# Optimization experiments

Measured on AMD Instinct MI355X. Metric: run time of the kernel, lower is better.

Reference implementation:

```python
import jax, jax.numpy as jnp
import numpy as np

N_NODES = 8192
GNN_DIM = 512
N_FEAT = 64
N_ITER = 4


def setup_inputs() -> dict:
    key = jax.random.key(0)
    ks = jax.random.split(key, 8)
    scale = 1.0 / np.sqrt(GNN_DIM)
    return {
        "labels": jax.random.normal(ks[0], (N_NODES, GNN_DIM), dtype=jnp.float32),
        "adj": jax.random.uniform(ks[1], (N_NODES, N_NODES), dtype=jnp.float32),
        "features": jax.random.normal(ks[2], (N_FEAT,), dtype=jnp.float32),
        "W_self": jax.random.normal(ks[3], (GNN_DIM, GNN_DIM), dtype=jnp.float32) * scale,
        "b_self": jax.random.normal(ks[4], (GNN_DIM,), dtype=jnp.float32) * scale,
        "W_neigh": jax.random.normal(ks[5], (GNN_DIM, GNN_DIM), dtype=jnp.float32) * scale,
        "W_fc": jax.random.normal(ks[6], (1, GNN_DIM + N_FEAT), dtype=jnp.float32) * scale,
        "b_fc": jax.random.normal(ks[7], (1,), dtype=jnp.float32) * scale,
    }


def reference(labels, adj, features, W_self, b_self, W_neigh, W_fc, b_fc):
    x = labels  # [N, D]
    for _ in range(N_ITER):
        acc = adj @ x                                   # [N, D] neighbor aggregation
        x = jax.nn.relu(x @ W_self.T + b_self + acc @ W_neigh.T)
    pooled = jnp.mean(x, axis=0)                        # [D]
    z = jnp.concatenate([pooled, features]) @ W_fc.T + b_fc  # [1]
    return jax.nn.sigmoid(z)
```

## Files before the change

kernel.cpp:

```cpp
#include <hip/hip_runtime.h>

typedef __bf16 bf16;
typedef bf16 bf16x8 __attribute__((ext_vector_type(8)));
typedef bf16 bf16x4 __attribute__((ext_vector_type(4)));
typedef float f32x4 __attribute__((ext_vector_type(4)));
typedef int i32x4 __attribute__((ext_vector_type(4)));
typedef unsigned int u32;
typedef unsigned int u32x4 __attribute__((ext_vector_type(4)));
typedef unsigned char u8;
typedef unsigned long long u64;

constexpr int NN = 8192;
constexpr int DD = 512;
constexpr size_t PSZB = (size_t)NN * DD * 2;
constexpr size_t PSZE = (size_t)NN * DD;
constexpr int NS = 4;

static __device__ inline bf16x8 cvt8(const float* __restrict__ p) {
  f32x4 a = *(const f32x4*)p;
  f32x4 b = *(const f32x4*)(p + 4);
  bf16x8 r;
  r[0] = (bf16)a[0]; r[1] = (bf16)a[1]; r[2] = (bf16)a[2]; r[3] = (bf16)a[3];
  r[4] = (bf16)b[0]; r[5] = (bf16)b[1]; r[6] = (bf16)b[2]; r[7] = (bf16)b[3];
  return r;
}

static __device__ inline u32 pk4_i8(f32x4 v) {
  u32 b0 = (u32)((int)__builtin_rintf(v[0])) & 255u;
  u32 b1 = (u32)((int)__builtin_rintf(v[1])) & 255u;
  u32 b2 = (u32)((int)__builtin_rintf(v[2])) & 255u;
  u32 b3 = (u32)((int)__builtin_rintf(v[3])) & 255u;
  return b0 | (b1 << 8) | (b2 << 16) | (b3 << 24);
}

#define GLDS(g, l) __builtin_amdgcn_global_load_lds( \
    (const __attribute__((address_space(1))) unsigned int*)(const void*)(g), \
    (__attribute__((address_space(3))) unsigned int*)(void*)(l), 16, 0, 0)


__global__ __launch_bounds__(256) void convert_w_kernel(
    const float* __restrict__ a, const float* __restrict__ b,
    bf16* __restrict__ ao, bf16* __restrict__ bo, float* __restrict__ pooled) {
  int tid = (int)threadIdx.x;
  if (blockIdx.x == 0) {
    pooled[tid] = 0.f;
    pooled[tid + 256] = 0.f;
  }
  int i8 = ((int)blockIdx.x * 256 + tid) * 8;
  if (i8 < DD * DD) {
    *(bf16x8*)&ao[i8] = cvt8(a + i8);
  } else {
    int j = i8 - DD * DD;
    *(bf16x8*)&bo[j] = cvt8(b + j);
  }
}

__global__ __launch_bounds__(256) void convert_adj_kernel(
    const float* __restrict__ a, u8* __restrict__ o) {
  size_t i16 = ((size_t)blockIdx.x * 256 + threadIdx.x) * 16;
  const float* p = a + i16;
  u32x4 w;
#pragma unroll
  for (int q = 0; q < 4; ++q) {
    f32x4 v = *(const f32x4*)(p + 4 * q);
    v *= 127.f;
    w[q] = pk4_i8(v);
  }
  *(u32x4*)(o + i16) = w;
}

__global__ __launch_bounds__(256) void convert_x_kernel(
    const float* __restrict__ src, bf16* __restrict__ xb, u8* __restrict__ xbT8) {
  __shared__ __align__(16) float tile[64][68];
  const int tid = (int)threadIdx.x;
  const int r0 = (int)blockIdx.x * 64;
  const int c0 = (int)blockIdx.y * 64;
#pragma unroll
  for (int p = 0; p < 4; ++p) {
    int row = p * 16 + (tid >> 4);
    int col = (tid & 15) * 4;
    *(f32x4*)&tile[row][col] = *(const f32x4*)&src[(size_t)(r0 + row) * DD + c0 + col];
  }
  __syncthreads();
#pragma unroll
  for (int p = 0; p < 4; ++p) {
    int row = p * 16 + (tid >> 4);
    int col = (tid & 15) * 4;
    f32x4 v = *(const f32x4*)&tile[row][col];
    bf16x4 o;
    o[0] = (bf16)v[0]; o[1] = (bf16)v[1]; o[2] = (bf16)v[2]; o[3] = (bf16)v[3];
    *(bf16x4*)&xb[(size_t)(r0 + row) * DD + c0 + col] = o;
  }
  {
    int c = tid >> 2;
    int rp = (tid & 3) * 16;
    u32x4 w;
#pragma unroll
    for (int q = 0; q < 4; ++q) {
      f32x4 v;
#pragma unroll
      for (int j = 0; j < 4; ++j) v[j] = tile[rp + 4 * q + j][c] * 16.f;
      w[q] = pk4_i8(v);
    }
    *(u32x4*)&xbT8[(size_t)(c0 + c) * NN + r0 + rp] = w;
  }
}


__device__ __forceinline__ void stage_half8(const u8* __restrict__ g, int grow0, int k0b,
                                            u8* smbase, int wave, int lane) {
  int row = grow0 + wave * 16 + (lane >> 2);
  int col = k0b + (((lane & 3) ^ ((lane >> 2) & 3)) << 4);
  GLDS(g + (size_t)row * NN + col, smbase + wave * 1024);
}

__global__ __launch_bounds__(512, 4)
void gemm1_kernel(const u8* __restrict__ adjb, const u8* __restrict__ xbT8,
                  bf16* __restrict__ pbase) {
  __shared__ __align__(16) u8 sm[49152];
  const int bid  = (int)blockIdx.x;
  const int xcd  = bid & 7;
  const int p    = bid >> 3;
  const int s    = xcd >> 1;
  const int cb   = xcd & 1;
  const int prow0 = p * 128;
  const int bcol0 = cb * 256;
  const int kb    = s * 2048;
  bf16* __restrict__ P = pbase + (size_t)s * PSZE;

  const int tid  = (int)threadIdx.x;
  const int lane = tid & 63;
  const int wave = tid >> 6;
  const int wr   = wave >> 2;
  const int wc   = wave & 3;
  const int fr   = lane & 15, fq = lane >> 4;

  i32x4 acc[4][4] = {};

#define A_OFF(par) ((par) * 24576)
#define B_OFF(par) ((par) * 24576 + 8192)
#define STAGE_A(tile, par) \
  stage_half8(adjb, prow0, kb + ((tile) & 31) * 64, sm + A_OFF(par), wave, lane)
#define STAGE_B(tile, half, par) \
  stage_half8(xbT8, bcol0 + (half) * 128, kb + ((tile) & 31) * 64, \
              sm + B_OFF(par) + (half) * 8192, wave, lane)
#define BARRIER() __builtin_amdgcn_s_barrier(); __builtin_amdgcn_sched_barrier(0)

  STAGE_B(0, 0, 0); STAGE_B(0, 1, 0); STAGE_A(0, 0);
  STAGE_B(1, 0, 1); STAGE_B(1, 1, 1);

  i32x4 bvp[4], afp[2];

#define LOAD_B(par)                                                        \
  _Pragma("unroll") for (int n = 0; n < 4; ++n) {                          \
    int rowl = wc * 64 + n * 16 + fr;                                      \
    int slot = fq ^ (rowl & 3);                                            \
    bvp[n] = *(const i32x4*)&sm[B_OFF(par) + rowl * 64 + slot * 16];       \
  }
#define LOAD_A2(qb, par)                                                   \
  _Pragma("unroll") for (int j = 0; j < 2; ++j) {                          \
    int rowl = wr * 64 + ((qb) + j) * 16 + fr;                             \
    int slot = fq ^ (rowl & 3);                                            \
    afp[j] = *(const i32x4*)&sm[A_OFF(par) + rowl * 64 + slot * 16];       \
  }
#define HMFMA(qb)                                                          \
  __builtin_amdgcn_s_setprio(1);                                           \
  _Pragma("unroll") for (int j = 0; j < 2; ++j)                            \
  _Pragma("unroll") for (int n = 0; n < 4; ++n)                            \
    acc[(qb) + j][n] = __builtin_amdgcn_mfma_i32_16x16x64_i8(              \
        afp[j], bvp[n], acc[(qb) + j][n], 0, 0, 0);                        \
  __builtin_amdgcn_s_setprio(0);

  int par = 0;
  for (int t = 0; t < 32; ++t, par ^= 1) {
    asm volatile("s_waitcnt vmcnt(2)" ::: "memory");
    BARRIER();
    LOAD_B(par);
    LOAD_A2(0, par);
    STAGE_A(t + 1, par ^ 1);
    HMFMA(0);
    BARRIER();
    LOAD_A2(2, par);
    STAGE_B(t + 2, 0, par);
    STAGE_B(t + 2, 1, par);
    HMFMA(2);
  }

#pragma unroll
  for (int m = 0; m < 4; ++m)
#pragma unroll
    for (int n = 0; n < 4; ++n)
#pragma unroll
      for (int r = 0; r < 4; ++r) {
        int row = prow0 + wr * 64 + m * 16 + fq * 4 + r;
        int col = bcol0 + wc * 64 + n * 16 + fr;
        P[(size_t)row * DD + col] = (bf16)(float)acc[m][n][r];
      }
#undef A_OFF
#undef B_OFF
#undef STAGE_A
#undef STAGE_B
#undef LOAD_B
#undef LOAD_A2
#undef HMFMA
#undef BARRIER
}

__global__ __launch_bounds__(1024, 4)
void gemm2_kernel(const bf16* __restrict__ wsb, const bf16* __restrict__ wnb,
                  bf16* __restrict__ xb, const bf16* __restrict__ pbase,
                  const float* __restrict__ bself, u8* __restrict__ xbT8,
                  float* __restrict__ pooled, int dopool,
                  float alpha, float inv_bn) {
  __shared__ __align__(16) char smem[139264];
  const int tid  = (int)threadIdx.x;
  const int lane = tid & 63;
  const int wave = tid >> 6;
  const int n0 = (int)blockIdx.x * 32;
  const int fr = lane & 15, fq = lane >> 4;
  const int srow = lane >> 3;
  const int scol = ((lane & 7) ^ (srow & 7)) * 8;
  const int fnode = tid >> 3, fks = tid & 7;

  f32x4 acc[2][2] = {};

  {
    bf16* la = (bf16*)smem;
#pragma unroll
    for (int c = 0; c < 4; ++c) {
      int chunk = wave * 4 + c;
      GLDS(wsb + (size_t)(chunk * 8 + srow) * DD + scol, &la[chunk * 512]);
    }
    if (wave < 4)
      GLDS(xb + (size_t)(n0 + wave * 8 + srow) * DD + scol,
           &((bf16*)(smem + 131072))[wave * 512]);
  }
  asm volatile("s_waitcnt vmcnt(0)" ::: "memory");
  __builtin_amdgcn_s_barrier();

  for (int t = 0; t < 16; ++t) {
    const int par = t & 1;
    bf16* la = (bf16*)(smem + par * 65536);
    bf16* lb = (bf16*)(smem + 131072 + par * 4096);

    bf16x8 fv0, fv1, fv2, fv3;
    bool fold = false;
    if (t < 15) {
      const int tn = t + 1, prn = tn >> 3, k0n = (tn & 7) * 64;
      const bf16* __restrict__ An = prn ? wnb : wsb;
      bf16* lan = (bf16*)(smem + (par ^ 1) * 65536);
#pragma unroll
      for (int c = 0; c < 4; ++c) {
        int chunk = wave * 4 + c;
        GLDS(An + (size_t)(chunk * 8 + srow) * DD + k0n + scol, &lan[chunk * 512]);
      }
      if (prn == 0) {
        if (wave < 4)
          GLDS(xb + (size_t)(n0 + wave * 8 + srow) * DD + k0n + scol,
               &((bf16*)(smem + 131072 + (par ^ 1) * 4096))[wave * 512]);
      } else if (tid < 256) {
        fold = true;
        const bf16* p0 = pbase + (size_t)(n0 + fnode) * DD + k0n + fks * 8;
        fv0 = *(const bf16x8*)(p0);
        fv1 = *(const bf16x8*)(p0 + PSZE);
        fv2 = *(const bf16x8*)(p0 + 2 * PSZE);
        fv3 = *(const bf16x8*)(p0 + 3 * PSZE);
      }
    }

    bf16x8 af[2][2], bv[2][2];
#pragma unroll
    for (int kk = 0; kk < 2; ++kk) {
#pragma unroll
      for (int m = 0; m < 2; ++m) {
        int rowl = wave * 32 + m * 16 + fr;
        int slot = (kk * 4 + fq) ^ (rowl & 7);
        af[kk][m] = *(const bf16x8*)&la[rowl * 64 + slot * 8];
      }
#pragma unroll
      for (int n = 0; n < 2; ++n) {
        int rowl = n * 16 + fr;
        int slot = (kk * 4 + fq) ^ (rowl & 7);
        bv[kk][n] = *(const bf16x8*)&lb[rowl * 64 + slot * 8];
      }
    }
#pragma unroll
    for (int kk = 0; kk < 2; ++kk)
#pragma unroll
      for (int m = 0; m < 2; ++m)
#pragma unroll
        for (int n = 0; n < 2; ++n)
          acc[m][n] = __builtin_amdgcn_mfma_f32_16x16x32_bf16(af[kk][m], bv[kk][n], acc[m][n], 0, 0, 0);

    if (fold) {
      bf16x8 o;
#pragma unroll
      for (int j = 0; j < 8; ++j)
        o[j] = (bf16)(((float)fv0[j] + (float)fv1[j] + (float)fv2[j] + (float)fv3[j]) * alpha);
      *(bf16x8*)&((bf16*)(smem + 131072 + (par ^ 1) * 4096))[fnode * 64 + (fks ^ (fnode & 7)) * 8] = o;
    }

    asm volatile("s_waitcnt vmcnt(0) lgkmcnt(0)" ::: "memory");
    __builtin_amdgcn_s_barrier();
  }

  if (dopool) {
#pragma unroll
    for (int m = 0; m < 2; ++m)
#pragma unroll
      for (int r = 0; r < 4; ++r) {
        int d = wave * 32 + m * 16 + fq * 4 + r;
        float b = bself[d];
        float v0 = acc[m][0][r] + b, v1 = acc[m][1][r] + b;
        float sv = (v0 > 0.f ? v0 : 0.f) + (v1 > 0.f ? v1 : 0.f);
        sv += __shfl_xor(sv, 1);
        sv += __shfl_xor(sv, 2);
        sv += __shfl_xor(sv, 4);
        sv += __shfl_xor(sv, 8);
        if (fr == 0) atomicAdd(&pooled[d], sv);
      }
    return;
  }

  bf16* lds_t = (bf16*)smem;
  u8*   lds8  = (u8*)(smem + 40960);
#pragma unroll
  for (int m = 0; m < 2; ++m)
#pragma unroll
    for (int n = 0; n < 2; ++n)
#pragma unroll
      for (int r = 0; r < 4; ++r) {
        int d = wave * 32 + m * 16 + fq * 4 + r;
        int node = n * 16 + fr;
        float v = acc[m][n][r] + bself[d];
        v = v > 0.f ? v : 0.f;
        lds_t[node * 520 + d] = (bf16)v;
        lds8[d * 32 + node] = (u8)(int)__builtin_rintf(fminf(v * inv_bn, 127.f));
      }
  __syncthreads();
  {
    int node = tid >> 5;
    int dc = (tid & 31) * 16;
    bf16x8 v0 = *(const bf16x8*)&lds_t[node * 520 + dc];
    bf16x8 v1 = *(const bf16x8*)&lds_t[node * 520 + dc + 8];
    *(bf16x8*)&xb[(size_t)(n0 + node) * DD + dc] = v0;
    *(bf16x8*)&xb[(size_t)(n0 + node) * DD + dc + 8] = v1;
  }
  {
    int d = tid >> 1, half = tid & 1;
    u32x4 w = *(const u32x4*)&lds8[d * 32 + half * 16];
    *(u32x4*)&xbT8[(size_t)d * NN + n0 + half * 16] = w;
  }
}


__global__ __launch_bounds__(64) void final_kernel(
    const float* __restrict__ pooled, const float* __restrict__ features,
    const float* __restrict__ wfc, const float* __restrict__ bfc,
    float* __restrict__ out) {
  const int t = (int)threadIdx.x;
  float s = 0.f;
  for (int i = t; i < DD + 64; i += 64) {
    float v = (i < DD) ? pooled[i] * (1.0f / (float)NN) : features[i - DD];
    s += v * wfc[i];
  }
#pragma unroll
  for (int off = 32; off > 0; off >>= 1) s += __shfl_down(s, off);
  if (t == 0) {
    float z = s + bfc[0];
    out[0] = 1.0f / (1.0f + expf(-z));
  }
}


extern "C" void kernel_launch(void* const* d_in, const int* in_sizes, int n_in,
                              void* d_out, int out_size, void* d_ws, size_t ws_size,
                              hipStream_t stream) {
  const float* labels   = (const float*)d_in[0];
  const float* adj      = (const float*)d_in[1];
  const float* features = (const float*)d_in[2];
  const float* W_self   = (const float*)d_in[3];
  const float* b_self   = (const float*)d_in[4];
  const float* W_neigh  = (const float*)d_in[5];
  const float* W_fc     = (const float*)d_in[6];
  const float* b_fc     = (const float*)d_in[7];
  float* out = (float*)d_out;

  const float BETA[5] = {1.f / 16.f, 16.f, 8192.f, 16777216.f, 1.f};

  char* ws = (char*)d_ws;
  bf16*  xb    = (bf16*)(ws);
  u8*    xbT8  = (u8*)(ws + PSZB);
  bf16*  pbase = (bf16*)(ws + 2 * PSZB);
  char*  after_p = ws + (size_t)(2 + NS) * PSZB;
  bf16*  wsb    = (bf16*)(after_p);
  bf16*  wnb    = (bf16*)(after_p + 524288);
  float* pooled = (float*)(after_p + 1048576);
  u8*    adjb8  = (u8*)(after_p + 1048576 + 4096);

  convert_w_kernel<<<2 * DD * DD / 8 / 256, 256, 0, stream>>>(W_self, W_neigh, wsb, wnb, pooled);
  convert_adj_kernel<<<(int)((size_t)NN * NN / 16 / 256), 256, 0, stream>>>(adj, adjb8);
  convert_x_kernel<<<dim3(NN / 64, DD / 64), 256, 0, stream>>>(labels, xb, xbT8);

  for (int it = 0; it < 4; ++it) {
    gemm1_kernel<<<512, 512, 0, stream>>>(adjb8, xbT8, pbase);
    gemm2_kernel<<<NN / 32, 1024, 0, stream>>>(wsb, wnb, xb, pbase, b_self, xbT8,
                                               pooled, it == 3 ? 1 : 0,
                                               BETA[it] * (1.f / 127.f),
                                               1.f / BETA[it + 1]);
  }

  final_kernel<<<1, 64, 0, stream>>>(pooled, features, W_fc, b_fc, out);
}
```

Baseline: 347.8 us.

## Triple-buffer B tiles in gemm1 and issue all MFMAs per k-step in one phase

Restructures the gemm1 int8 main loop so B tiles rotate through three LDS buffers while A stays double-buffered. All four A fragments are loaded at once and all 16 MFMAs run in a single block. Both global-to-LDS stages are issued before the MFMAs, which removes the mid-iteration split. LDS use grows from 48 KB to 64 KB per block, which may lower occupancy, and register pressure rises.

```diff
diff --git a/kernel.cpp b/kernel.cpp
--- a/kernel.cpp
+++ b/kernel.cpp
@@ -117,7 +117,7 @@
 __global__ __launch_bounds__(512, 4)
 void gemm1_kernel(const u8* __restrict__ adjb, const u8* __restrict__ xbT8,
                   bf16* __restrict__ pbase) {
-  __shared__ __align__(16) u8 sm[49152];
+  __shared__ __align__(16) u8 sm[65536];
   const int bid  = (int)blockIdx.x;
   const int xcd  = bid & 7;
   const int p    = bid >> 3;
@@ -137,53 +137,56 @@
 
   i32x4 acc[4][4] = {};
 
-#define A_OFF(par) ((par) * 24576)
-#define B_OFF(par) ((par) * 24576 + 8192)
-#define STAGE_A(tile, par) \
-  stage_half8(adjb, prow0, kb + ((tile) & 31) * 64, sm + A_OFF(par), wave, lane)
-#define STAGE_B(tile, half, par) \
+#define A_OFF(pa) ((pa) * 8192)
+#define B_OFF(b3) (16384 + (b3) * 16384)
+#define STAGE_A(tile, pa) \
+  stage_half8(adjb, prow0, kb + ((tile) & 31) * 64, sm + A_OFF(pa), wave, lane)
+#define STAGE_B(tile, half, b3) \
   stage_half8(xbT8, bcol0 + (half) * 128, kb + ((tile) & 31) * 64, \
-              sm + B_OFF(par) + (half) * 8192, wave, lane)
+              sm + B_OFF(b3) + (half) * 8192, wave, lane)
 #define BARRIER() __builtin_amdgcn_s_barrier(); __builtin_amdgcn_sched_barrier(0)
 
   STAGE_B(0, 0, 0); STAGE_B(0, 1, 0); STAGE_A(0, 0);
   STAGE_B(1, 0, 1); STAGE_B(1, 1, 1);
 
-  i32x4 bvp[4], afp[2];
-
-#define LOAD_B(par)                                                        \
+  i32x4 bvp[4], afp[4];
+
+#define LOAD_B(b3)                                                         \
   _Pragma("unroll") for (int n = 0; n < 4; ++n) {                          \
     int rowl = wc * 64 + n * 16 + fr;                                      \
     int slot = fq ^ (rowl & 3);                                            \
-    bvp[n] = *(const i32x4*)&sm[B_OFF(par) + rowl * 64 + slot * 16];       \
-  }
-#define LOAD_A2(qb, par)                                                   \
-  _Pragma("unroll") for (int j = 0; j < 2; ++j) {                          \
-    int rowl = wr * 64 + ((qb) + j) * 16 + fr;                             \
+    bvp[n] = *(const i32x4*)&sm[B_OFF(b3) + rowl * 64 + slot * 16];        \
+  }
+#define LOAD_A4(pa)                                                        \
+  _Pragma("unroll") for (int j = 0; j < 4; ++j) {                          \
+    int rowl = wr * 64 + j * 16 + fr;                                      \
     int slot = fq ^ (rowl & 3);                                            \
-    afp[j] = *(const i32x4*)&sm[A_OFF(par) + rowl * 64 + slot * 16];       \
-  }
-#define HMFMA(qb)                                                          \
+    afp[j] = *(const i32x4*)&sm[A_OFF(pa) + rowl * 64 + slot * 16];        \
+  }
+#define TMFMA()                                                            \
   __builtin_amdgcn_s_setprio(1);                                           \
-  _Pragma("unroll") for (int j = 0; j < 2; ++j)                            \
+  _Pragma("unroll") for (int j = 0; j < 4; ++j)                            \
   _Pragma("unroll") for (int n = 0; n < 4; ++n)                            \
-    acc[(qb) + j][n] = __builtin_amdgcn_mfma_i32_16x16x64_i8(              \
-        afp[j], bvp[n], acc[(qb) + j][n], 0, 0, 0);                        \
+    acc[j][n] = __builtin_amdgcn_mfma_i32_16x16x64_i8(                     \
+        afp[j], bvp[n], acc[j][n], 0, 0, 0);                               \
   __builtin_amdgcn_s_setprio(0);
 
-  int par = 0;
-  for (int t = 0; t < 32; ++t, par ^= 1) {
+  int parA = 0, bufB = 0;
+  for (int t = 0; t < 32; ++t) {
     asm volatile("s_waitcnt vmcnt(2)" ::: "memory");
     BARRIER();
-    LOAD_B(par);
-    LOAD_A2(0, par);
-    STAGE_A(t + 1, par ^ 1);
-    HMFMA(0);
+    LOAD_B(bufB);
+    LOAD_A4(parA);
+    STAGE_A(t + 1, parA ^ 1);
+    {
+      int b2 = bufB == 0 ? 2 : bufB - 1;
+      STAGE_B(t + 2, 0, b2);
+      STAGE_B(t + 2, 1, b2);
+    }
+    TMFMA();
     BARRIER();
-    LOAD_A2(2, par);
-    STAGE_B(t + 2, 0, par);
-    STAGE_B(t + 2, 1, par);
-    HMFMA(2);
+    parA ^= 1;
+    bufB = bufB == 2 ? 0 : bufB + 1;
   }
 
 #pragma unroll
@@ -201,8 +204,8 @@
 #undef STAGE_A
 #undef STAGE_B
 #undef LOAD_B
-#undef LOAD_A2
-#undef HMFMA
+#undef LOAD_A4
+#undef TMFMA
 #undef BARRIER
 }
 
```

New measurement: 351.5 us. Within noise of the previous version (+1.1%).
